# Kernel tuning notes

Hardware: AMD Instinct MI355X
Metric: run time of the kernel (lower is better)

## Reference

```python
import jax, jax.numpy as jnp
import numpy as np

B, T, C, H = 4, 2048, 1024, 16
HD = C // H

def setup_inputs() -> dict:
    key = jax.random.key(0)
    ks = jax.random.split(key, 9)
    s = 1.0 / np.sqrt(C)
    return {
        'x':  jax.random.normal(ks[0], (B, T, C), jnp.float32),
        'Wq': jax.random.normal(ks[1], (C, C), jnp.float32) * s,
        'bq': jnp.zeros((C,), jnp.float32),
        'Wk': jax.random.normal(ks[2], (C, C), jnp.float32) * s,
        'bk': jnp.zeros((C,), jnp.float32),
        'Wv': jax.random.normal(ks[3], (C, C), jnp.float32) * s,
        'bv': jnp.zeros((C,), jnp.float32),
        'Wo': jax.random.normal(ks[4], (C, C), jnp.float32) * s,
        'bo': jnp.zeros((C,), jnp.float32),
    }

def reference(x, Wq, bq, Wk, bk, Wv, bv, Wo, bo):
    Bx, Tx, Cx = x.shape
    # projections (torch Linear: x @ W.T + b); split heads -> (B,H,T,HD)
    def heads(y):
        return y.reshape(Bx, Tx, H, HD).transpose(0, 2, 1, 3)
    q = heads(x @ Wq.T + bq)
    k = heads(x @ Wk.T + bk)
    v = heads(x @ Wv.T + bv)
    # NOTE: original scales by 1/sqrt(embedding_dim), not head_dim
    scale = 1.0 / jnp.sqrt(jnp.asarray(Cx, x.dtype))
    att = jnp.einsum('bhqd,bhkd->bhqk', q, k) * scale
    mask = jnp.tril(jnp.ones((Tx, Tx), dtype=bool))
    att = jnp.where(mask, att, jnp.asarray(-jnp.inf, att.dtype))
    att = jax.nn.softmax(att, axis=-1)
    y = jnp.einsum('bhqk,bhkd->bhqd', att, v)
    y = y.transpose(0, 2, 1, 3).reshape(Bx, Tx, Cx)
    return y @ Wo.T + bo
```

## Files before the change

kernel.cpp:

```cpp
#include <hip/hip_runtime.h>
#include <hip/hip_bf16.h>
#include <stdint.h>

#define NB 4
#define NT 2048
#define NC 1024
#define NH 16
#define NHD 64
#define NM (NB*NT)

typedef __attribute__((ext_vector_type(8))) __bf16 bf16x8;
typedef __attribute__((ext_vector_type(4))) float floatx4;
typedef __attribute__((ext_vector_type(8))) unsigned short ushortx8;

#define AS1(p) ((const __attribute__((address_space(1))) void*)(p))
#define AS3(p) ((__attribute__((address_space(3))) void*)(p))

__device__ __forceinline__ unsigned short f2bf(float f) {
    union { float f; unsigned int u; } v; v.f = f;
    unsigned int u = v.u;
    return (unsigned short)((u + 0x7FFFu + ((u >> 16) & 1u)) >> 16);
}
__device__ __forceinline__ unsigned int pk2(float lo, float hi) {
    union { float f; unsigned int u; } a, b; a.f = hi; b.f = lo;
    return __builtin_amdgcn_perm(a.u, b.u, 0x07060302u);
}


__global__ void cast_all(const float* __restrict__ x,
                         const float* __restrict__ w0, const float* __restrict__ w1,
                         const float* __restrict__ w2, const float* __restrict__ w3,
                         unsigned short* __restrict__ xo,
                         unsigned short* __restrict__ o0, unsigned short* __restrict__ o1,
                         unsigned short* __restrict__ o2, unsigned short* __restrict__ o3)
{
    const int wid  = (blockIdx.x * blockDim.x + threadIdx.x) >> 6;
    const int lane = threadIdx.x & 63;
    const float* in; unsigned short* out; int tile;
    if (wid < 16384) { in = x; out = xo; tile = wid; }
    else {
        const int t = wid - 16384;
        tile = t & 2047;
        switch (t >> 11) {
            case 0: in = w0; out = o0; break;
            case 1: in = w1; out = o1; break;
            case 2: in = w2; out = o2; break;
            default: in = w3; out = o3; break;
        }
    }
    const int R = tile >> 5, C = tile & 31;
    const float* src = in + ((size_t)(R*16 + (lane >> 2)))*1024 + C*32 + (lane & 3)*8;
    const floatx4 v0 = *(const floatx4*)src;
    const floatx4 v1 = *(const floatx4*)(src + 4);
    ushortx8 o;
    o[0] = f2bf(v0[0]); o[1] = f2bf(v0[1]); o[2] = f2bf(v0[2]); o[3] = f2bf(v0[3]);
    o[4] = f2bf(v1[0]); o[5] = f2bf(v1[1]); o[6] = f2bf(v1[2]); o[7] = f2bf(v1[3]);
    *(ushortx8*)&out[(size_t)tile*512 + (((lane & 3)*16 + (lane >> 2)))*8] = o;
}

#define TM 128
#define TN 128
#define BK 32

template<int MODE>
__device__ __forceinline__ void gemm_core(
    const unsigned short* __restrict__ A,
    const unsigned short* __restrict__ W,
    const float* __restrict__ bias,
    void* __restrict__ Out,
    unsigned short* As, unsigned short* Bs,
    int m_base, int n_base, float oscale)
{
    const int tid  = threadIdx.x;
    const int lane = tid & 63;
    const int wv   = tid >> 6;
    const int quad = lane >> 4;
    const int l16  = lane & 15;
    const int wm = (wv >> 1) * 64;
    const int wn = (wv & 1) * 64;

    floatx4 acc[4][4];
    #pragma unroll
    for (int i = 0; i < 4; ++i)
        #pragma unroll
        for (int j = 0; j < 4; ++j)
            acc[i][j] = (floatx4){0.f, 0.f, 0.f, 0.f};

    const int kct = NC >> 5;

    const unsigned short* At = A + ((size_t)((m_base >> 4) + wv*2) * kct) * 512 + (size_t)lane*8;
    const unsigned short* Wt = W + ((size_t)((n_base >> 4) + wv*2) * kct) * 512 + (size_t)lane*8;
    const size_t rstride = (size_t)kct * 512;

    #pragma unroll
    for (int i = 0; i < 2; ++i) {
        __builtin_amdgcn_global_load_lds(AS1(At + i*rstride),
                                         AS3(&As[(wv*2 + i)*512]), 16, 0, 0);
        __builtin_amdgcn_global_load_lds(AS1(Wt + i*rstride),
                                         AS3(&Bs[(wv*2 + i)*512]), 16, 0, 0);
    }

    #pragma unroll 1
    for (int kt = 0; kt < 32; ++kt) {
        const int cur = (kt & 1) << 12;
        const int nxt = 4096 - cur;
        if (kt < 31) {
            #pragma unroll
            for (int i = 0; i < 2; ++i) {
                __builtin_amdgcn_global_load_lds(
                    AS1(At + (size_t)(kt+1)*512 + i*rstride),
                    AS3(&As[nxt + (wv*2 + i)*512]), 16, 0, 0);
                __builtin_amdgcn_global_load_lds(
                    AS1(Wt + (size_t)(kt+1)*512 + i*rstride),
                    AS3(&Bs[nxt + (wv*2 + i)*512]), 16, 0, 0);
            }
            asm volatile("s_waitcnt vmcnt(4)" ::: "memory");
        } else {
            asm volatile("s_waitcnt vmcnt(0)" ::: "memory");
        }
        __builtin_amdgcn_s_barrier();

        bf16x8 af[4], bfr[4];
        #pragma unroll
        for (int mi = 0; mi < 4; ++mi)
            af[mi] = *(const bf16x8*)&As[cur + ((wv >> 1)*4 + mi)*512 + lane*8];
        #pragma unroll
        for (int ni = 0; ni < 4; ++ni)
            bfr[ni] = *(const bf16x8*)&Bs[cur + ((wv & 1)*4 + ni)*512 + lane*8];

        #pragma unroll
        for (int mi = 0; mi < 4; ++mi)
            #pragma unroll
            for (int ni = 0; ni < 4; ++ni) {
                if (MODE == 1)
                    acc[mi][ni] = __builtin_amdgcn_mfma_f32_16x16x32_bf16(
                        bfr[ni], af[mi], acc[mi][ni], 0, 0, 0);
                else
                    acc[mi][ni] = __builtin_amdgcn_mfma_f32_16x16x32_bf16(
                        af[mi], bfr[ni], acc[mi][ni], 0, 0, 0);
            }
        __builtin_amdgcn_s_barrier();
    }

    #pragma unroll
    for (int mi = 0; mi < 4; ++mi) {
        #pragma unroll
        for (int ni = 0; ni < 4; ++ni) {
            if (MODE == 0) {
                const int col = n_base + wn + ni*16 + l16;
                const float bv = bias[col & 1023];
                #pragma unroll
                for (int r = 0; r < 4; ++r) {
                    const int row = m_base + wm + mi*16 + quad*4 + r;
                    ((float*)Out)[(size_t)row * NC + col] =
                        (acc[mi][ni][r] + bv) * oscale;
                }
            } else if (MODE == 1) {
                const int d0 = n_base + wn + ni*16 + quad*4;
                const int t  = m_base + wm + mi*16 + l16;
                const float4 b4 = *(const float4*)&bias[d0];
                const int bb = t >> 11, tt = t & (NT - 1);
                const int h  = (d0 >> 6) & (NH - 1), dd0 = d0 & 63;
                const int bh = bb * NH + h;
                const size_t idx0 =
                    ((size_t)((bh*128 + (tt >> 4))*2 + (dd0 >> 5)))*512
                    + (size_t)((((dd0 >> 3) & 3)*16 + (tt & 15))*8 + (dd0 & 7));
                ushort4 st;
                st.x = f2bf((acc[mi][ni][0] + b4.x) * oscale);
                st.y = f2bf((acc[mi][ni][1] + b4.y) * oscale);
                st.z = f2bf((acc[mi][ni][2] + b4.z) * oscale);
                st.w = f2bf((acc[mi][ni][3] + b4.w) * oscale);
                *(ushort4*)&((unsigned short*)Out)[idx0] = st;
            } else {
                const int col = n_base + wn + ni*16 + l16;
                const float bv = bias[col & 1023];
                const int row0 = m_base + wm + mi*16 + quad*4;
                const int bb = row0 >> 11, t0 = row0 & (NT - 1);
                const int h  = (col >> 6) & (NH - 1), hd = col & 63;
                const int bh = bb * NH + h;
                const int tk0 = t0 & 31;
                const int qv  = (tk0 >> 2) & 3;
                const int jv0 = (tk0 >> 4) << 2;
                const size_t idx0 =
                    ((size_t)((bh*64 + (t0 >> 5))*4 + (hd >> 4)))*512
                    + (size_t)((qv*16 + (hd & 15))*8 + jv0);
                ushort4 st;
                st.x = f2bf((acc[mi][ni][0] + bv) * oscale);
                st.y = f2bf((acc[mi][ni][1] + bv) * oscale);
                st.z = f2bf((acc[mi][ni][2] + bv) * oscale);
                st.w = f2bf((acc[mi][ni][3] + bv) * oscale);
                *(ushort4*)&((unsigned short*)Out)[idx0] = st;
            }
        }
    }
}

#define QSCALE (0.03125f * 1.44269504088896340736f)

__global__ __launch_bounds__(256) void gemm_qkv(
    const unsigned short* __restrict__ A,
    const unsigned short* __restrict__ Wq, const unsigned short* __restrict__ Wk,
    const unsigned short* __restrict__ Wv,
    const float* __restrict__ bq, const float* __restrict__ bk,
    const float* __restrict__ bv,
    unsigned short* __restrict__ Qo, unsigned short* __restrict__ Ko,
    unsigned short* __restrict__ Vo)
{
    __shared__ __align__(16) unsigned short As[2*TM*BK];
    __shared__ __align__(16) unsigned short Bs[2*TN*BK];
    const int wi = blockIdx.y >> 3;
    const int n_base = (blockIdx.y & 7) * TN;
    const int m_base = blockIdx.x * TM;
    if (wi == 0)
        gemm_core<1>(A, Wq, bq, Qo, As, Bs, m_base, n_base, QSCALE);
    else if (wi == 1)
        gemm_core<1>(A, Wk, bk, Ko, As, Bs, m_base, n_base, 1.0f);
    else
        gemm_core<2>(A, Wv, bv, Vo, As, Bs, m_base, n_base, 1.0f);
}

__global__ __launch_bounds__(256) void gemm_out(
    const unsigned short* __restrict__ A,
    const unsigned short* __restrict__ W,
    const float* __restrict__ bias,
    float* __restrict__ Out)
{
    __shared__ __align__(16) unsigned short As[2*TM*BK];
    __shared__ __align__(16) unsigned short Bs[2*TN*BK];
    gemm_core<0>(A, W, bias, Out, As, Bs, blockIdx.x * TM, blockIdx.y * TN, 1.0f);
}

__device__ __forceinline__ void attn_tile(
    const bf16x8 kf[4][2], const bf16x8 vf[4][2],
    const bf16x8 q[4], floatx4 o[2][4], float l[2],
    bool diag, bool skiphi, int q0, int j0, int quad, int l16)
{
    #pragma unroll
    for (int sub = 0; sub < 2; ++sub) {
        const bf16x8 qx0 = q[sub*2];
        const bf16x8 qx1 = q[sub*2 + 1];

        floatx4 s[4];
        __builtin_amdgcn_s_setprio(1);
        #pragma unroll
        for (int ct = 0; ct < 2; ++ct) {
            s[ct] = (floatx4){0.f,0.f,0.f,0.f};
            s[ct] = __builtin_amdgcn_mfma_f32_16x16x32_bf16(kf[ct][0], qx0, s[ct], 0,0,0);
            s[ct] = __builtin_amdgcn_mfma_f32_16x16x32_bf16(kf[ct][1], qx1, s[ct], 0,0,0);
        }
        if (!skiphi) {
            #pragma unroll
            for (int ct = 2; ct < 4; ++ct) {
                s[ct] = (floatx4){0.f,0.f,0.f,0.f};
                s[ct] = __builtin_amdgcn_mfma_f32_16x16x32_bf16(kf[ct][0], qx0, s[ct], 0,0,0);
                s[ct] = __builtin_amdgcn_mfma_f32_16x16x32_bf16(kf[ct][1], qx1, s[ct], 0,0,0);
            }
        }
        __builtin_amdgcn_s_setprio(0);

        float p[4][4];
        float lsum = 0.f;
        const int row = q0 + sub*16 + l16;
        if (!diag) {
            #pragma unroll
            for (int ct = 0; ct < 2; ++ct)
                #pragma unroll
                for (int r = 0; r < 4; ++r) {
                    p[ct][r] = __builtin_amdgcn_exp2f(s[ct][r]);
                    lsum += p[ct][r];
                }
        } else {
            #pragma unroll
            for (int ct = 0; ct < 2; ++ct)
                #pragma unroll
                for (int r = 0; r < 4; ++r) {
                    const int key = j0 + ct*16 + quad*4 + r;
                    p[ct][r] = (key <= row) ? __builtin_amdgcn_exp2f(s[ct][r]) : 0.f;
                    lsum += p[ct][r];
                }
        }
        if (!skiphi) {
            if (!diag) {
                #pragma unroll
                for (int ct = 2; ct < 4; ++ct)
                    #pragma unroll
                    for (int r = 0; r < 4; ++r) {
                        p[ct][r] = __builtin_amdgcn_exp2f(s[ct][r]);
                        lsum += p[ct][r];
                    }
            } else {
                #pragma unroll
                for (int ct = 2; ct < 4; ++ct)
                    #pragma unroll
                    for (int r = 0; r < 4; ++r) {
                        const int key = j0 + ct*16 + quad*4 + r;
                        p[ct][r] = (key <= row) ? __builtin_amdgcn_exp2f(s[ct][r]) : 0.f;
                        lsum += p[ct][r];
                    }
            }
        }
        l[sub] += lsum;

        union { bf16x8 v; unsigned int u[4]; } pf0;
        pf0.u[0] = pk2(p[0][0], p[0][1]); pf0.u[1] = pk2(p[0][2], p[0][3]);
        pf0.u[2] = pk2(p[1][0], p[1][1]); pf0.u[3] = pk2(p[1][2], p[1][3]);

        __builtin_amdgcn_s_setprio(1);
        #pragma unroll
        for (int nt = 0; nt < 4; ++nt)
            o[sub][nt] = __builtin_amdgcn_mfma_f32_16x16x32_bf16(vf[nt][0], pf0.v, o[sub][nt], 0,0,0);
        __builtin_amdgcn_s_setprio(0);

        if (!skiphi) {
            union { bf16x8 v; unsigned int u[4]; } pf1;
            pf1.u[0] = pk2(p[2][0], p[2][1]); pf1.u[1] = pk2(p[2][2], p[2][3]);
            pf1.u[2] = pk2(p[3][0], p[3][1]); pf1.u[3] = pk2(p[3][2], p[3][3]);
            __builtin_amdgcn_s_setprio(1);
            #pragma unroll
            for (int nt = 0; nt < 4; ++nt)
                o[sub][nt] = __builtin_amdgcn_mfma_f32_16x16x32_bf16(vf[nt][1], pf1.v, o[sub][nt], 0,0,0);
            __builtin_amdgcn_s_setprio(0);
        }
    }
}

__device__ __forceinline__ void attn_store(
    unsigned short* __restrict__ Y, const floatx4 o[2][4], const float l[2],
    int q0, int b, int h, int quad, int l16)
{
    float la = l[0], lb = l[1];
    la += __shfl_xor(la, 16); la += __shfl_xor(la, 32);
    lb += __shfl_xor(lb, 16); lb += __shfl_xor(lb, 32);
    const float ia = 1.0f / la, ib = 1.0f / lb;
    const size_t Rbase = (size_t)((b*NT + q0) >> 4);
    const int cg = (quad >> 1), co = (quad & 1)*4;
    #pragma unroll
    for (int nt = 0; nt < 4; ++nt) {
        const size_t base = ((Rbase*32 + h*2 + (nt >> 1))*512)
                          + (size_t)((((nt & 1)*2 + cg)*16 + l16)*8 + co);
        ushort4 wa, wb;
        wa.x = f2bf(o[0][nt][0]*ia); wa.y = f2bf(o[0][nt][1]*ia);
        wa.z = f2bf(o[0][nt][2]*ia); wa.w = f2bf(o[0][nt][3]*ia);
        wb.x = f2bf(o[1][nt][0]*ib); wb.y = f2bf(o[1][nt][1]*ib);
        wb.z = f2bf(o[1][nt][2]*ib); wb.w = f2bf(o[1][nt][3]*ib);
        *(ushort4*)&Y[base]         = wa;
        *(ushort4*)&Y[base + 16384] = wb;
    }
}

__device__ __forceinline__ void attn_pair(
    const unsigned short* __restrict__ Qf,
    const unsigned short* __restrict__ Kf,
    const unsigned short* __restrict__ Vf,
    unsigned short* __restrict__ Y,
    int bh, int stA, int stB, int lane)
{
    const int quad = lane >> 4, l16 = lane & 15;
    const int b = bh >> 4, h = bh & (NH - 1);
    const int q0A = stA * 32, q0B = stB * 32;
    const int FA = q0A >> 6, FB = q0B >> 6;
    const bool skA = (q0A & 32) == 0;
    const bool skB = (q0B & 32) == 0;

    const size_t qbA = ((size_t)(bh*128 + stA*2))*1024 + (size_t)lane*8;
    const size_t qbB = ((size_t)(bh*128 + stB*2))*1024 + (size_t)lane*8;
    bf16x8 qA[4], qB[4];
    qA[0] = *(const bf16x8*)&Qf[qbA];
    qA[1] = *(const bf16x8*)&Qf[qbA + 512];
    qA[2] = *(const bf16x8*)&Qf[qbA + 1024];
    qA[3] = *(const bf16x8*)&Qf[qbA + 1536];
    qB[0] = *(const bf16x8*)&Qf[qbB];
    qB[1] = *(const bf16x8*)&Qf[qbB + 512];
    qB[2] = *(const bf16x8*)&Qf[qbB + 1024];
    qB[3] = *(const bf16x8*)&Qf[qbB + 1536];

    const unsigned short* kp = Kf + (size_t)bh*131072 + (size_t)lane*8;
    const unsigned short* vp = Vf + (size_t)bh*131072 + (size_t)lane*8;

    floatx4 oA[2][4], oB[2][4];
    float lA[2] = {0.f, 0.f}, lB[2] = {0.f, 0.f};
    #pragma unroll
    for (int s2 = 0; s2 < 2; ++s2)
        #pragma unroll
        for (int nt = 0; nt < 4; ++nt) {
            oA[s2][nt] = (floatx4){0.f,0.f,0.f,0.f};
            oB[s2][nt] = (floatx4){0.f,0.f,0.f,0.f};
        }

    for (int f = 0; f <= FB; ++f) {
        const int j0 = f * 64;
        bf16x8 kf[4][2], vf[4][2];
        const unsigned short* kt = kp + (size_t)f * 4096;
        #pragma unroll
        for (int ct = 0; ct < 4; ++ct) {
            kf[ct][0] = *(const bf16x8*)&kt[ct*1024];
            kf[ct][1] = *(const bf16x8*)&kt[ct*1024 + 512];
        }
        const unsigned short* vt = vp + (size_t)f * 4096;
        #pragma unroll
        for (int nt = 0; nt < 4; ++nt) {
            vf[nt][0] = *(const bf16x8*)&vt[nt*512];
            vf[nt][1] = *(const bf16x8*)&vt[2048 + nt*512];
        }

        if (f <= FA)
            attn_tile(kf, vf, qA, oA, lA, f == FA, (f == FA) && skA,
                      q0A, j0, quad, l16);
        attn_tile(kf, vf, qB, oB, lB, f == FB, (f == FB) && skB,
                  q0B, j0, quad, l16);
    }

    attn_store(Y, oA, lA, q0A, b, h, quad, l16);
    attn_store(Y, oB, lB, q0B, b, h, quad, l16);
}

__global__ __launch_bounds__(256, 2) void flash_attn(
    const unsigned short* __restrict__ Qf,
    const unsigned short* __restrict__ Kf,
    const unsigned short* __restrict__ Vf,
    unsigned short* __restrict__ Y)
{
    const int tid  = threadIdx.x;
    const int wave = tid >> 6;
    const int lane = tid & 63;
    const int L  = blockIdx.x;
    const int bh = (L & 7) * 8 + ((L >> 3) & 7);
    const int x  = L >> 6;
    const int w  = x * 4 + wave;
    attn_pair(Qf, Kf, Vf, Y, bh, w, 63 - w, lane);
}

extern "C" void kernel_launch(void* const* d_in, const int* in_sizes, int n_in,
                              void* d_out, int out_size, void* d_ws, size_t ws_size,
                              hipStream_t stream) {
    const float* x  = (const float*)d_in[0];
    const float* Wq = (const float*)d_in[1];
    const float* bq = (const float*)d_in[2];
    const float* Wk = (const float*)d_in[3];
    const float* bk = (const float*)d_in[4];
    const float* Wv = (const float*)d_in[5];
    const float* bv = (const float*)d_in[6];
    const float* Wo = (const float*)d_in[7];
    const float* bo = (const float*)d_in[8];

    char* ws = (char*)d_ws;
    size_t off = 0;
    auto alloc = [&](size_t bytes) -> void* {
        void* p = ws + off;
        off += (bytes + 255) & ~(size_t)255;
        return p;
    };
    unsigned short* xb  = (unsigned short*)alloc((size_t)NM * NC * 2);
    unsigned short* Wqb = (unsigned short*)alloc((size_t)NC * NC * 2);
    unsigned short* Wkb = (unsigned short*)alloc((size_t)NC * NC * 2);
    unsigned short* Wvb = (unsigned short*)alloc((size_t)NC * NC * 2);
    unsigned short* Wob = (unsigned short*)alloc((size_t)NC * NC * 2);
    unsigned short* Qb  = (unsigned short*)alloc((size_t)NM * NC * 2);
    unsigned short* Kb  = (unsigned short*)alloc((size_t)NM * NC * 2);
    unsigned short* Vtb = (unsigned short*)alloc((size_t)NM * NC * 2);
    unsigned short* Yb  = (unsigned short*)alloc((size_t)NM * NC * 2);

    cast_all<<<(24576*64)/256, 256, 0, stream>>>(
        x, Wq, Wk, Wv, Wo, xb, Wqb, Wkb, Wvb, Wob);

    gemm_qkv<<<dim3(NM / TM, 24), 256, 0, stream>>>(
        xb, Wqb, Wkb, Wvb, bq, bk, bv, Qb, Kb, Vtb);

    flash_attn<<<dim3(512), 256, 0, stream>>>(Qb, Kb, Vtb, Yb);

    gemm_out<<<dim3(NM / TM, NC / TN), 256, 0, stream>>>(Yb, Wob, bo, (float*)d_out);
}
```

Measured before the change: 233.8 us.

## Compute Q, K, V projections in one block and tree-reduce softmax row sums

Each QKV GEMM block now computes all three projections for its output tile in sequence instead of one projection per block, and the grid shrinks to a third. The intent is for the shared A tile of x to be reused from cache across the three weight matrices. It costs parallelism: fewer blocks, each doing three times the work. Separately, the softmax row-sum in the attention tile switches from a serial accumulation chain to a pairwise tree of partial sums, which shortens the dependency chain.

```diff
diff --git a/kernel.cpp b/kernel.cpp
--- a/kernel.cpp
+++ b/kernel.cpp
@@ -208,15 +208,11 @@
 {
     __shared__ __align__(16) unsigned short As[2*TM*BK];
     __shared__ __align__(16) unsigned short Bs[2*TN*BK];
-    const int wi = blockIdx.y >> 3;
-    const int n_base = (blockIdx.y & 7) * TN;
     const int m_base = blockIdx.x * TM;
-    if (wi == 0)
-        gemm_core<1>(A, Wq, bq, Qo, As, Bs, m_base, n_base, QSCALE);
-    else if (wi == 1)
-        gemm_core<1>(A, Wk, bk, Ko, As, Bs, m_base, n_base, 1.0f);
-    else
-        gemm_core<2>(A, Wv, bv, Vo, As, Bs, m_base, n_base, 1.0f);
+    const int n_base = blockIdx.y * TN;
+    gemm_core<1>(A, Wq, bq, Qo, As, Bs, m_base, n_base, QSCALE);
+    gemm_core<1>(A, Wk, bk, Ko, As, Bs, m_base, n_base, 1.0f);
+    gemm_core<2>(A, Wv, bv, Vo, As, Bs, m_base, n_base, 1.0f);
 }
 
 __global__ __launch_bounds__(256) void gemm_out(
@@ -259,47 +255,43 @@
         __builtin_amdgcn_s_setprio(0);
 
         float p[4][4];
-        float lsum = 0.f;
+        float psum[4];
         const int row = q0 + sub*16 + l16;
-        if (!diag) {
-            #pragma unroll
-            for (int ct = 0; ct < 2; ++ct)
+        #pragma unroll
+        for (int ct = 0; ct < 2; ++ct) {
+            if (!diag) {
                 #pragma unroll
-                for (int r = 0; r < 4; ++r) {
+                for (int r = 0; r < 4; ++r)
                     p[ct][r] = __builtin_amdgcn_exp2f(s[ct][r]);
-                    lsum += p[ct][r];
-                }
-        } else {
-            #pragma unroll
-            for (int ct = 0; ct < 2; ++ct)
+            } else {
                 #pragma unroll
                 for (int r = 0; r < 4; ++r) {
                     const int key = j0 + ct*16 + quad*4 + r;
                     p[ct][r] = (key <= row) ? __builtin_amdgcn_exp2f(s[ct][r]) : 0.f;
-                    lsum += p[ct][r];
                 }
+            }
+            psum[ct] = (p[ct][0] + p[ct][1]) + (p[ct][2] + p[ct][3]);
         }
         if (!skiphi) {
-            if (!diag) {
-                #pragma unroll
-                for (int ct = 2; ct < 4; ++ct)
+            #pragma unroll
+            for (int ct = 2; ct < 4; ++ct) {
+                if (!diag) {
                     #pragma unroll
-                    for (int r = 0; r < 4; ++r) {
+                    for (int r = 0; r < 4; ++r)
                         p[ct][r] = __builtin_amdgcn_exp2f(s[ct][r]);
-                        lsum += p[ct][r];
-                    }
-            } else {
-                #pragma unroll
-                for (int ct = 2; ct < 4; ++ct)
+                } else {
                     #pragma unroll
                     for (int r = 0; r < 4; ++r) {
                         const int key = j0 + ct*16 + quad*4 + r;
                         p[ct][r] = (key <= row) ? __builtin_amdgcn_exp2f(s[ct][r]) : 0.f;
-                        lsum += p[ct][r];
                     }
-            }
-        }
-        l[sub] += lsum;
+                }
+                psum[ct] = (p[ct][0] + p[ct][1]) + (p[ct][2] + p[ct][3]);
+            }
+            l[sub] += (psum[0] + psum[1]) + (psum[2] + psum[3]);
+        } else {
+            l[sub] += psum[0] + psum[1];
+        }
 
         union { bf16x8 v; unsigned int u[4]; } pf0;
         pf0.u[0] = pk2(p[0][0], p[0][1]); pf0.u[1] = pk2(p[0][2], p[0][3]);
@@ -463,7 +455,7 @@
     cast_all<<<(24576*64)/256, 256, 0, stream>>>(
         x, Wq, Wk, Wv, Wo, xb, Wqb, Wkb, Wvb, Wob);
 
-    gemm_qkv<<<dim3(NM / TM, 24), 256, 0, stream>>>(
+    gemm_qkv<<<dim3(NM / TM, NC / TN), 256, 0, stream>>>(
         xb, Wqb, Wkb, Wvb, bq, bk, bv, Qb, Kb, Vtb);
 
     flash_attn<<<dim3(512), 256, 0, stream>>>(Qb, Kb, Vtb, Yb);
```

Result: no change. 233.4 us (-0.1%).
